# Kernel tuning notes

Measured on AMD Instinct MI355X. Metric: run time of the kernel, lower is better.

The kernel has to match this reference:

```python
import jax, jax.numpy as jnp
import numpy as np


def _hard_sigmoid(x):
    # torch: clamp(0.2 * x + 0.5, 0, 1)
    return jnp.clip(0.2 * x + 0.5, 0.0, 1.0)


def _hardtanh(x):
    return jnp.clip(x, -1.0, 1.0)


def _run_dir(x, h0, c0, w_ih, w_hh, b):
    """One direction of a HardLSTM layer.
    x: [T, B, I], h0/c0: [B, H], w_ih: [4H, I], w_hh: [4H, H], b: [4H]
    (b is bias_ih + bias_hh of the original cell; identical math).
    """
    # Hoist the input projection out of the recurrence (one big GEMM).
    gx = jnp.einsum('tbi,gi->tbg', x, w_ih) + b  # [T, B, 4H]

    def step(carry, gx_t):
        h, c = carry
        gates = gx_t + h @ w_hh.T  # [B, 4H]
        i, f, g, o = jnp.split(gates, 4, axis=-1)
        i = _hard_sigmoid(i)
        f = _hard_sigmoid(f)
        g = _hardtanh(g)
        o = _hard_sigmoid(o)
        cy = f * c + i * g
        hy = o * _hardtanh(cy)
        return (hy, cy), hy

    (h, c), ys = jax.lax.scan(step, (h0, c0), gx)
    return ys, h, c


def _bidir_layer(x, h0, c0, w_ih, w_hh, b):
    """h0/c0: [2, B, H]; w_ih: [2, 4H, I]; w_hh: [2, 4H, H]; b: [2, 4H]."""
    yf, hf, cf = _run_dir(x, h0[0], c0[0], w_ih[0], w_hh[0], b[0])
    yb, hb, cb = _run_dir(x[::-1], h0[1], c0[1], w_ih[1], w_hh[1], b[1])
    yb = yb[::-1]
    # torch cat([yf.unsqueeze(2), yb.unsqueeze(2)], 2).view(T, B, 2H)
    y = jnp.concatenate([yf, yb], axis=-1)  # [T, B, 2H]
    return y, jnp.stack([hf, hb]), jnp.stack([cf, cb])


def reference(x, h0, c0, w_ih0, w_hh0, b0, w_ih1, w_hh1, b1):
    # Stacked 2-layer bidirectional HardLSTM, time-major input.
    y0, h_l0, c_l0 = _bidir_layer(x, h0[0:2], c0[0:2], w_ih0, w_hh0, b0)
    y1, h_l1, c_l1 = _bidir_layer(y0, h0[2:4], c0[2:4], w_ih1, w_hh1, b1)
    hn = jnp.concatenate([h_l0, h_l1], axis=0)  # [4, B, H]
    cn = jnp.concatenate([c_l0, c_l1], axis=0)
    return y1, hn, cn


def setup_inputs() -> dict:
    key = jax.random.key(0)
    ks = jax.random.split(key, 8)
    T, B, I, H = 512, 32, 512, 1024
    stdv = 1.0 / np.sqrt(H)  # matches reset_parameters uniform(-stdv, stdv) scale
    FGB = 1.0  # forget_gate_bias

    x = jax.random.normal(ks[0], (T, B, I), dtype=jnp.float32)
    h0 = jnp.zeros((4, B, H), dtype=jnp.float32)
    c0 = jnp.zeros((4, B, H), dtype=jnp.float32)

    def mk_w(k, shape):
        return (jax.random.normal(k, shape, dtype=jnp.float32) * stdv).astype(jnp.float32)

    w_ih0 = mk_w(ks[1], (2, 4 * H, I))
    w_hh0 = mk_w(ks[2], (2, 4 * H, H))
    b0 = mk_w(ks[3], (2, 4 * H))
    w_ih1 = mk_w(ks[4], (2, 4 * H, 2 * H))
    w_hh1 = mk_w(ks[5], (2, 4 * H, H))
    b1 = mk_w(ks[6], (2, 4 * H))
    # forget gate bias override (bias_ih forget slice = FGB, bias_hh = 0 -> sum = FGB)
    b0 = b0.at[:, H:2 * H].set(FGB)
    b1 = b1.at[:, H:2 * H].set(FGB)

    return {"x": x, "h0": h0, "c0": c0,
            "w_ih0": w_ih0, "w_hh0": w_hh0, "b0": b0,
            "w_ih1": w_ih1, "w_hh1": w_hh1, "b1": b1}
```

## Files before the change

### kernel.cpp

```cpp
#include <hip/hip_runtime.h>
#include <cstdint>


typedef _Float16 half8 __attribute__((ext_vector_type(8)));
typedef _Float16 half4v __attribute__((ext_vector_type(4)));
typedef float floatx4 __attribute__((ext_vector_type(4)));
typedef int int4v __attribute__((ext_vector_type(4)));

#define T_LEN 512
#define BATCH 32
#define HID 1024
#define NTB 16384
#define UPW 16
#define WPD 64

__device__ __forceinline__ float hsig(float x) {
  return fminf(fmaxf(fmaf(0.2f, x, 0.5f), 0.0f), 1.0f);
}
__device__ __forceinline__ float htanh(float x) {
  return fminf(fmaxf(x, -1.0f), 1.0f);
}

__device__ __forceinline__ int4v load_co16(const void* p) {
  int4v r;
  asm volatile("global_load_dwordx4 %0, %1, off sc0 sc1"
               : "=&v"(r) : "v"(p) : "memory");
  return r;
}
__device__ __forceinline__ void store_co16(void* p, int4v v) {
  asm volatile("global_store_dwordx4 %0, %1, off sc0 sc1"
               :: "v"(p), "v"(v) : "memory");
}
__device__ __forceinline__ void waitcnt0() {
  asm volatile("s_waitcnt vmcnt(0)" ::: "memory");
}

__device__ __forceinline__ void gll16(const void* g, void* l) {
  __builtin_amdgcn_global_load_lds((const __attribute__((address_space(1))) void*)g,
                                   (__attribute__((address_space(3))) void*)l,
                                   16, 0, 0);
}

__global__ __launch_bounds__(256) void cvt_f32_f16(const float* __restrict__ s,
                                                   _Float16* __restrict__ d,
                                                   int n4) {
  int i = blockIdx.x * blockDim.x + threadIdx.x;
  int stride = gridDim.x * blockDim.x;
  for (; i < n4; i += stride) {
    float4 v = ((const float4*)s)[i];
    half4v h = {(_Float16)v.x, (_Float16)v.y, (_Float16)v.z, (_Float16)v.w};
    ((half4v*)d)[i] = h;
  }
}

__global__ __launch_bounds__(256) void gemm_gx(const _Float16* __restrict__ A,
                                               const _Float16* __restrict__ B,
                                               const float* __restrict__ bias,
                                               _Float16* __restrict__ C,
                                               int K) {
  __shared__ __align__(16) _Float16 A_s[128 * 64];
  __shared__ __align__(16) _Float16 B_s[128 * 64];
  const int tid = threadIdx.x;
  const int lane = tid & 63;
  const int w = tid >> 6;
  const int bm = blockIdx.x >> 7;
  const int bn = blockIdx.x & 127;
  const int m0 = bm * 128, n0 = bn * 128;

  floatx4 acc[4][4] = {};

  const int srow = w * 8 + (lane >> 3);
  const int scol = ((lane & 7) ^ ((lane >> 3) & 7)) * 8;
  const _Float16* Ag = A + (size_t)(m0 + srow) * K + scol;
  const _Float16* Bg = B + (size_t)(n0 + srow) * K + scol;
  char* As_base = (char*)A_s + (size_t)(w * 8) * 128;
  char* Bs_base = (char*)B_s + (size_t)(w * 8) * 128;

  const int wm = (w >> 1) * 64;
  const int wn = (w & 1) * 64;
  const int fr = lane & 15;
  const int fk = lane >> 4;

  for (int kb = 0; kb < K; kb += 64) {
#pragma unroll
    for (int i = 0; i < 4; ++i) {
      gll16(Ag + (size_t)i * 32 * K + kb, As_base + i * 32 * 128);
      gll16(Bg + (size_t)i * 32 * K + kb, Bs_base + i * 32 * 128);
    }
    __syncthreads();
#pragma unroll
    for (int kt = 0; kt < 2; ++kt) {
      half8 af[4], bf[4];
#pragma unroll
      for (int mi = 0; mi < 4; ++mi) {
        int row = wm + mi * 16 + fr;
        int k8 = kt * 4 + fk;
        af[mi] = *(const half8*)(A_s + row * 64 + ((k8 ^ (row & 7)) << 3));
      }
#pragma unroll
      for (int ni = 0; ni < 4; ++ni) {
        int row = wn + ni * 16 + fr;
        int k8 = kt * 4 + fk;
        bf[ni] = *(const half8*)(B_s + row * 64 + ((k8 ^ (row & 7)) << 3));
      }
#pragma unroll
      for (int mi = 0; mi < 4; ++mi)
#pragma unroll
        for (int ni = 0; ni < 4; ++ni)
          acc[mi][ni] = __builtin_amdgcn_mfma_f32_16x16x32_f16(af[mi], bf[ni],
                                                               acc[mi][ni], 0, 0, 0);
    }
    __syncthreads();
  }

#pragma unroll
  for (int mi = 0; mi < 4; ++mi) {
    int rowb = m0 + wm + mi * 16 + fk * 4;
#pragma unroll
    for (int r = 0; r < 4; ++r) {
      float bv = bias[rowb + r];
#pragma unroll
      for (int ni = 0; ni < 4; ++ni) {
        int col = n0 + wn + ni * 16 + fr;
        C[(size_t)(rowb + r) * NTB + col] = (_Float16)(acc[mi][ni][r] + bv);
      }
    }
  }
}

__global__ __launch_bounds__(512) void recur(const _Float16* __restrict__ gx,
                                             const _Float16* __restrict__ whh,
                                             const float* __restrict__ h0,
                                             const float* __restrict__ c0,
                                             _Float16* __restrict__ hbuf,
                                             int* __restrict__ flags,
                                             int layer,
                                             _Float16* __restrict__ yf16,
                                             float* __restrict__ yf32,
                                             float* __restrict__ hn,
                                             float* __restrict__ cn) {
  __shared__ __align__(16) _Float16 h_s[BATCH * HID];
  __shared__ float gates_s[64 * 33];
  __shared__ __align__(16) _Float16 hout_s[BATCH * UPW];

  const int tid = threadIdx.x;
  const int lane = tid & 63;
  const int w = tid >> 6;
  const int g = w >> 1;
  const int wn = w & 1;
  const int dir = blockIdx.x >> 6;
  const int wgd = blockIdx.x & 63;
  const int u0 = wgd * UPW;
  const int fr = lane & 15, fk = lane >> 4;

  half8 af[32];
  {
    const _Float16* wrow = whh + ((size_t)dir * 4096 + g * 1024 + u0 + fr) * HID;
#pragma unroll
    for (int kt = 0; kt < 32; ++kt)
      af[kt] = *(const half8*)(wrow + kt * 32 + fk * 8);
  }

  const int eb = tid & 31, eu = tid >> 5;
  const size_t st0 = (size_t)(layer * 2 + dir) * (BATCH * HID);
  float c = c0[st0 + eb * HID + u0 + eu];

  _Float16* buf0 = hbuf + (size_t)dir * (BATCH * HID);
  _Float16* buf1 = hbuf + (size_t)(2 + dir) * (BATCH * HID);
  int* fl = flags + dir * WPD;

  hout_s[eb * UPW + eu] = (_Float16)h0[st0 + eb * HID + u0 + eu];
  __syncthreads();
  if (w == 0) {
    int b = lane >> 1, hf = lane & 1;
    int4v v = *(const int4v*)(hout_s + b * UPW + hf * 8);
    store_co16(buf0 + (size_t)b * HID + u0 + hf * 8, v);
    waitcnt0();
    if (lane == 0) {
      int fv = 1;
      asm volatile("global_store_dword %0, %1, off sc0 sc1"
                   :: "v"(fl + wgd), "v"(fv) : "memory");
    }
  }

  const size_t GS = (size_t)1024 * NTB;
  const _Float16* gxb = gx + ((size_t)dir * 4096 + u0 + eu) * NTB;

  for (int t = 0; t < T_LEN; ++t) {
    if (w == 0) {
      const int want = t + 1;
      for (;;) {
        int v;
        asm volatile("global_load_dword %0, %1, off sc0 sc1\n\ts_waitcnt vmcnt(0)"
                     : "=&v"(v) : "v"(fl + lane) : "memory");
        if (__all(v >= want)) break;
        __builtin_amdgcn_s_sleep(1);
      }
    }
    __syncthreads();

    const _Float16* src = (t & 1) ? buf1 : buf0;
    _Float16* dst = (t & 1) ? buf0 : buf1;

    int4v hv[8];
#pragma unroll
    for (int i = 0; i < 8; ++i)
      hv[i] = load_co16((const char*)src + (size_t)(i * 512 + tid) * 16);
    waitcnt0();
#pragma unroll
    for (int i = 0; i < 8; ++i) {
      int cbyte = (i * 512 + tid) * 16;
      int b = cbyte >> 11;
      int slot = cbyte & 2047;
      *(int4v*)((char*)h_s + b * 2048 + (slot ^ ((b & 7) << 4))) = hv[i];
    }

    const int tseq = dir ? (T_LEN - 1 - t) : t;
    const size_t col = (size_t)tseq * BATCH + eb;
    float gxi = (float)gxb[0 * GS + col];
    float gxf = (float)gxb[1 * GS + col];
    float gxg = (float)gxb[2 * GS + col];
    float gxo = (float)gxb[3 * GS + col];

    __syncthreads();

    floatx4 acc0 = {0.f, 0.f, 0.f, 0.f}, acc1 = {0.f, 0.f, 0.f, 0.f};
    {
      const int b = wn * 16 + fr;
      const char* hp = (const char*)h_s + b * 2048;
      const int bx = (b & 7) << 4;
#pragma unroll
      for (int kt = 0; kt < 32; kt += 2) {
        half8 b0 = *(const half8*)(hp + ((kt * 64 + fk * 16) ^ bx));
        half8 b1 = *(const half8*)(hp + (((kt + 1) * 64 + fk * 16) ^ bx));
        acc0 = __builtin_amdgcn_mfma_f32_16x16x32_f16(af[kt], b0, acc0, 0, 0, 0);
        acc1 = __builtin_amdgcn_mfma_f32_16x16x32_f16(af[kt + 1], b1, acc1, 0, 0, 0);
      }
    }
    floatx4 acc = acc0 + acc1;
#pragma unroll
    for (int r = 0; r < 4; ++r)
      gates_s[(g * 16 + fk * 4 + r) * 33 + wn * 16 + fr] = acc[r];
    __syncthreads();

    float ip = gates_s[(0 * 16 + eu) * 33 + eb] + gxi;
    float fp = gates_s[(1 * 16 + eu) * 33 + eb] + gxf;
    float gp = gates_s[(2 * 16 + eu) * 33 + eb] + gxg;
    float op = gates_s[(3 * 16 + eu) * 33 + eb] + gxo;
    float ig = hsig(ip), fg = hsig(fp), gg = htanh(gp), og = hsig(op);
    c = fg * c + ig * gg;
    float h = og * htanh(c);

    size_t yidx = ((size_t)tseq * BATCH + eb) * 2048 + (size_t)dir * 1024 + u0 + eu;
    if (yf16) yf16[yidx] = (_Float16)h;
    else      yf32[yidx] = h;

    hout_s[eb * UPW + eu] = (_Float16)h;

    if (t == T_LEN - 1) {
      size_t o = st0 + eb * HID + u0 + eu;
      hn[o] = h;
      cn[o] = c;
    } else {
      __syncthreads();
      if (w == 0) {
        int b = lane >> 1, hf = lane & 1;
        int4v v = *(const int4v*)(hout_s + b * UPW + hf * 8);
        store_co16(dst + (size_t)b * HID + u0 + hf * 8, v);
        waitcnt0();
        if (lane == 0) {
          int fv = t + 2;
          asm volatile("global_store_dword %0, %1, off sc0 sc1"
                       :: "v"(fl + wgd), "v"(fv) : "memory");
        }
      }
    }
  }
}

extern "C" void kernel_launch(void* const* d_in, const int* in_sizes, int n_in,
                              void* d_out, int out_size, void* d_ws, size_t ws_size,
                              hipStream_t stream) {
  const float* x    = (const float*)d_in[0];
  const float* h0   = (const float*)d_in[1];
  const float* c0   = (const float*)d_in[2];
  const float* wih0 = (const float*)d_in[3];
  const float* whh0 = (const float*)d_in[4];
  const float* b0   = (const float*)d_in[5];
  const float* wih1 = (const float*)d_in[6];
  const float* whh1 = (const float*)d_in[7];
  const float* b1   = (const float*)d_in[8];
  float* out = (float*)d_out;

  char* ws = (char*)d_ws;
  size_t off = 0;
  int* flags = (int*)ws;                      off += 4096;
  _Float16* xh    = (_Float16*)(ws + off);    off += (size_t)8388608 * 2;
  _Float16* wih0h = (_Float16*)(ws + off);    off += (size_t)4194304 * 2;
  _Float16* whh0h = (_Float16*)(ws + off);    off += (size_t)8388608 * 2;
  _Float16* wih1h = (_Float16*)(ws + off);    off += (size_t)16777216 * 2;
  _Float16* whh1h = (_Float16*)(ws + off);    off += (size_t)8388608 * 2;
  _Float16* y0h   = (_Float16*)(ws + off);    off += (size_t)33554432 * 2;
  _Float16* hbuf  = (_Float16*)(ws + off);    off += (size_t)131072 * 2;
  _Float16* gxbuf = (_Float16*)(ws + off);    off += (size_t)134217728 * 2;

  hipMemsetAsync(flags, 0, 4096, stream);

  cvt_f32_f16<<<2048, 256, 0, stream>>>(x,    xh,    8388608 / 4);
  cvt_f32_f16<<<2048, 256, 0, stream>>>(wih0, wih0h, 4194304 / 4);
  cvt_f32_f16<<<2048, 256, 0, stream>>>(whh0, whh0h, 8388608 / 4);
  cvt_f32_f16<<<2048, 256, 0, stream>>>(wih1, wih1h, 16777216 / 4);
  cvt_f32_f16<<<2048, 256, 0, stream>>>(whh1, whh1h, 8388608 / 4);

  float* hn = out + 33554432;
  float* cn = out + 33685504;

  gemm_gx<<<8192, 256, 0, stream>>>(wih0h, xh, b0, gxbuf, 512);
  recur<<<128, 512, 0, stream>>>(gxbuf, whh0h, h0, c0, hbuf, flags, 0,
                                 y0h, nullptr, hn, cn);
  gemm_gx<<<8192, 256, 0, stream>>>(wih1h, y0h, b1, gxbuf, 2048);
  recur<<<128, 512, 0, stream>>>(gxbuf, whh1h, h0, c0, hbuf, flags + 128, 1,
                                 nullptr, out, hn, cn);
}
```

Before: 6.651 ms.

## Remap W_hh rows to keep gates in-wave, drop LDS gate exchange and barriers

Reorders the W_hh rows each wave loads so that all four gates of a unit land in the same wave's MFMA output. They are then exchanged with cross-lane shuffles instead of passing through a shared-memory gates buffer and an extra block barrier. Every wave now polls the flags itself, which removes the barrier after the spin-wait. The gx values for the next timestep are prefetched one iteration ahead, and __syncthreads is replaced by a lighter s_barrier that waits only on lgkmcnt. The cost is more global flag polling traffic from all waves, and correctness now relies on the hand-placed waitcnts being enough.

```diff
diff --git a/kernel.cpp b/kernel.cpp
--- a/kernel.cpp
+++ b/kernel.cpp
@@ -33,6 +33,12 @@
 }
 __device__ __forceinline__ void waitcnt0() {
   asm volatile("s_waitcnt vmcnt(0)" ::: "memory");
+}
+__device__ __forceinline__ void barrier_lgkm() {
+  asm volatile("s_waitcnt lgkmcnt(0)" ::: "memory");
+  __builtin_amdgcn_sched_barrier(0);
+  __builtin_amdgcn_s_barrier();
+  __builtin_amdgcn_sched_barrier(0);
 }
 
 __device__ __forceinline__ void gll16(const void* g, void* l) {
@@ -140,14 +146,12 @@
                                              float* __restrict__ hn,
                                              float* __restrict__ cn) {
   __shared__ __align__(16) _Float16 h_s[BATCH * HID];
-  __shared__ float gates_s[64 * 33];
   __shared__ __align__(16) _Float16 hout_s[BATCH * UPW];
 
   const int tid = threadIdx.x;
   const int lane = tid & 63;
   const int w = tid >> 6;
-  const int g = w >> 1;
-  const int wn = w & 1;
+  const int wu = w >> 1, wn = w & 1;
   const int dir = blockIdx.x >> 6;
   const int wgd = blockIdx.x & 63;
   const int u0 = wgd * UPW;
@@ -155,21 +159,23 @@
 
   half8 af[32];
   {
-    const _Float16* wrow = whh + ((size_t)dir * 4096 + g * 1024 + u0 + fr) * HID;
+    const int g = fr >> 2, du = fr & 3;
+    const _Float16* wrow = whh + ((size_t)dir * 4096 + g * 1024 + u0 + wu * 4 + du) * HID;
 #pragma unroll
     for (int kt = 0; kt < 32; ++kt)
       af[kt] = *(const half8*)(wrow + kt * 32 + fk * 8);
   }
 
-  const int eb = tid & 31, eu = tid >> 5;
+  const int unit = u0 + wu * 4 + fk;
+  const int bat  = wn * 16 + fr;
   const size_t st0 = (size_t)(layer * 2 + dir) * (BATCH * HID);
-  float c = c0[st0 + eb * HID + u0 + eu];
+  float c = c0[st0 + (size_t)bat * HID + unit];
 
   _Float16* buf0 = hbuf + (size_t)dir * (BATCH * HID);
   _Float16* buf1 = hbuf + (size_t)(2 + dir) * (BATCH * HID);
   int* fl = flags + dir * WPD;
 
-  hout_s[eb * UPW + eu] = (_Float16)h0[st0 + eb * HID + u0 + eu];
+  hout_s[bat * UPW + wu * 4 + fk] = (_Float16)h0[st0 + (size_t)bat * HID + unit];
   __syncthreads();
   if (w == 0) {
     int b = lane >> 1, hf = lane & 1;
@@ -184,10 +190,18 @@
   }
 
   const size_t GS = (size_t)1024 * NTB;
-  const _Float16* gxb = gx + ((size_t)dir * 4096 + u0 + eu) * NTB;
+  const _Float16* gxp = gx + ((size_t)dir * 4096 + unit) * NTB;
+
+  int ts0 = dir ? (T_LEN - 1) : 0;
+  float gxi = (float)gxp[0 * GS + (size_t)ts0 * BATCH + bat];
+  float gxf = (float)gxp[1 * GS + (size_t)ts0 * BATCH + bat];
+  float gxg = (float)gxp[2 * GS + (size_t)ts0 * BATCH + bat];
+  float gxo = (float)gxp[3 * GS + (size_t)ts0 * BATCH + bat];
+
+  const bool i1 = (fk >> 1) & 1, i0 = fk & 1;
 
   for (int t = 0; t < T_LEN; ++t) {
-    if (w == 0) {
+    {
       const int want = t + 1;
       for (;;) {
         int v;
@@ -197,7 +211,6 @@
         __builtin_amdgcn_s_sleep(1);
       }
     }
-    __syncthreads();
 
     const _Float16* src = (t & 1) ? buf1 : buf0;
     _Float16* dst = (t & 1) ? buf0 : buf1;
@@ -215,20 +228,19 @@
       *(int4v*)((char*)h_s + b * 2048 + (slot ^ ((b & 7) << 4))) = hv[i];
     }
 
-    const int tseq = dir ? (T_LEN - 1 - t) : t;
-    const size_t col = (size_t)tseq * BATCH + eb;
-    float gxi = (float)gxb[0 * GS + col];
-    float gxf = (float)gxb[1 * GS + col];
-    float gxg = (float)gxb[2 * GS + col];
-    float gxo = (float)gxb[3 * GS + col];
-
-    __syncthreads();
+    int tn = (t + 1 < T_LEN) ? t + 1 : t;
+    int tsn = dir ? (T_LEN - 1 - tn) : tn;
+    float ngxi = (float)gxp[0 * GS + (size_t)tsn * BATCH + bat];
+    float ngxf = (float)gxp[1 * GS + (size_t)tsn * BATCH + bat];
+    float ngxg = (float)gxp[2 * GS + (size_t)tsn * BATCH + bat];
+    float ngxo = (float)gxp[3 * GS + (size_t)tsn * BATCH + bat];
+
+    barrier_lgkm();
 
     floatx4 acc0 = {0.f, 0.f, 0.f, 0.f}, acc1 = {0.f, 0.f, 0.f, 0.f};
     {
-      const int b = wn * 16 + fr;
-      const char* hp = (const char*)h_s + b * 2048;
-      const int bx = (b & 7) << 4;
+      const char* hp = (const char*)h_s + bat * 2048;
+      const int bx = (bat & 7) << 4;
 #pragma unroll
       for (int kt = 0; kt < 32; kt += 2) {
         half8 b0 = *(const half8*)(hp + ((kt * 64 + fk * 16) ^ bx));
@@ -237,36 +249,42 @@
         acc1 = __builtin_amdgcn_mfma_f32_16x16x32_f16(af[kt + 1], b1, acc1, 0, 0, 0);
       }
     }
-    floatx4 acc = acc0 + acc1;
-#pragma unroll
-    for (int r = 0; r < 4; ++r)
-      gates_s[(g * 16 + fk * 4 + r) * 33 + wn * 16 + fr] = acc[r];
-    __syncthreads();
-
-    float ip = gates_s[(0 * 16 + eu) * 33 + eb] + gxi;
-    float fp = gates_s[(1 * 16 + eu) * 33 + eb] + gxf;
-    float gp = gates_s[(2 * 16 + eu) * 33 + eb] + gxg;
-    float op = gates_s[(3 * 16 + eu) * 33 + eb] + gxo;
-    float ig = hsig(ip), fg = hsig(fp), gg = htanh(gp), og = hsig(op);
+    floatx4 v = acc0 + acc1;
+    float s0 = i1 ? v[0] : v[2], s1 = i1 ? v[1] : v[3];
+    float r0 = __shfl_xor(s0, 32), r1 = __shfl_xor(s1, 32);
+    float A0 = i1 ? r0 : v[0], A1 = i1 ? r1 : v[1];
+    float A2 = i1 ? v[2] : r0, A3 = i1 ? v[3] : r1;
+    s0 = i0 ? A0 : A1; s1 = i0 ? A2 : A3;
+    r0 = __shfl_xor(s0, 16); r1 = __shfl_xor(s1, 16);
+    float gI = i0 ? r0 : A0, gF = i0 ? A1 : r0;
+    float gG = i0 ? r1 : A2, gO = i0 ? A3 : r1;
+
+    float ig = hsig(gI + gxi);
+    float fg = hsig(gF + gxf);
+    float gg = htanh(gG + gxg);
+    float og = hsig(gO + gxo);
     c = fg * c + ig * gg;
     float h = og * htanh(c);
 
-    size_t yidx = ((size_t)tseq * BATCH + eb) * 2048 + (size_t)dir * 1024 + u0 + eu;
+    hout_s[bat * UPW + wu * 4 + fk] = (_Float16)h;
+
+    const int tseq = dir ? (T_LEN - 1 - t) : t;
+    size_t yidx = ((size_t)tseq * BATCH + bat) * 2048 + (size_t)dir * 1024 + unit;
     if (yf16) yf16[yidx] = (_Float16)h;
     else      yf32[yidx] = h;
 
-    hout_s[eb * UPW + eu] = (_Float16)h;
+    gxi = ngxi; gxf = ngxf; gxg = ngxg; gxo = ngxo;
 
     if (t == T_LEN - 1) {
-      size_t o = st0 + eb * HID + u0 + eu;
+      size_t o = st0 + (size_t)bat * HID + unit;
       hn[o] = h;
       cn[o] = c;
     } else {
-      __syncthreads();
+      barrier_lgkm();
       if (w == 0) {
         int b = lane >> 1, hf = lane & 1;
-        int4v v = *(const int4v*)(hout_s + b * UPW + hf * 8);
-        store_co16(dst + (size_t)b * HID + u0 + hf * 8, v);
+        int4v vv = *(const int4v*)(hout_s + b * UPW + hf * 8);
+        store_co16(dst + (size_t)b * HID + u0 + hf * 8, vv);
         waitcnt0();
         if (lane == 0) {
           int fv = t + 2;
```

After: 7.533 ms. 13.3% more time.
